# Optimization experiments

Measured on AMD Instinct MI355X. Metric: run time of the kernel, lower is better.

Reference implementation:

```python
import jax, jax.numpy as jnp
import numpy as np

EPS = 1e-08
ROUTING_ITERS = 3

def squash(s, axis=-1):
    norm = jnp.linalg.norm(s, axis=axis, keepdims=True)
    return norm / (1.0 + norm ** 2 + EPS) * s

def setup_inputs() -> dict:
    key = jax.random.key(0)
    k1, k2, k3 = jax.random.split(key, 3)
    B, R, C, O, I = 512, 640, 10, 16, 8
    x = jax.random.normal(k1, (B, R, I), dtype=jnp.float32)
    W = jax.random.normal(k2, (R, C, O, I), dtype=jnp.float32) * 0.01
    bias = jax.random.uniform(k3, (1, 1, C, O), dtype=jnp.float32) * 0.01
    return {"x": x, "W": W, "bias": bias}

def reference(x, W, bias):
    # u_hat[b,r,c,o] = sum_i W[r,c,o,i] * x[b,r,i]
    u_hat = jnp.einsum('rcoi,bri->brco', W, x)  # [B,R,C,O]
    u_hat_d = jax.lax.stop_gradient(u_hat)
    B, R, C, _ = u_hat.shape
    b_ij = jnp.zeros((B, R, C, 1), dtype=u_hat.dtype)
    v_j = None
    for itr in range(ROUTING_ITERS):
        c_ij = jax.nn.softmax(b_ij, axis=2)               # softmax over capsules
        s_j = jnp.sum(c_ij * u_hat_d, axis=1, keepdims=True) + bias  # [B,1,C,O]
        v_j = squash(s_j, axis=-1)
        if itr < ROUTING_ITERS - 1:
            a_ij = jnp.sum(u_hat * v_j, axis=-1, keepdims=True)  # agreement, non-detached
            b_ij = b_ij + a_ij
    return jnp.squeeze(v_j, axis=1)  # [B,C,O]
```

## Files before the change

### kernel.cpp

```cpp
#include <hip/hip_runtime.h>
#include <hip/hip_cooperative_groups.h>
#include <math.h>

namespace cg = cooperative_groups;

#define BB 512
#define RR 640
#define CC 10
#define OO 16
#define CO 160
#define II 8
#define S_FLOATS (BB*CO)

#define ZCH (RR*CO)
#define LSTR 165

#define CG_NRG 16
#define CG_RPW 10

#define FB_NRG 32
#define FB_RPW 5

using f16x8 = __attribute__((ext_vector_type(8))) _Float16;
using f32x4 = __attribute__((ext_vector_type(4))) float;



__device__ __forceinline__ float exp_small(float a) {
    float f = __builtin_fmaf(a, 0.16666667f, 0.5f);
    f = __builtin_fmaf(a, f, 1.0f);
    return __builtin_fmaf(a, f, 1.0f);
}

__device__ __forceinline__ float rowsum16(float v) {
    int t;
    t = __builtin_amdgcn_update_dpp(0, __float_as_int(v), 0x128, 0xF, 0xF, true);
    v += __int_as_float(t);
    t = __builtin_amdgcn_update_dpp(0, __float_as_int(v), 0x124, 0xF, 0xF, true);
    v += __int_as_float(t);
    t = __builtin_amdgcn_update_dpp(0, __float_as_int(v), 0x122, 0xF, 0xF, true);
    v += __int_as_float(t);
    t = __builtin_amdgcn_update_dpp(0, __float_as_int(v), 0x121, 0xF, 0xF, true);
    v += __int_as_float(t);
    return v;
}


__global__ __launch_bounds__(256) void prep(const float* __restrict__ W,
                                            const float* __restrict__ x,
                                            _Float16* __restrict__ wf,
                                            _Float16* __restrict__ xf) {
    const int t = blockIdx.x * 256 + threadIdx.x;
    if (t < RR * CO * II) wf[t] = (_Float16)W[t];
    if (t < 16) wf[RR * CO * II + t] = (_Float16)0.f;
    const int i = t & 7;
    const int b = (t >> 3) & 511;
    const int r = t >> 12;
    xf[t] = (_Float16)x[((size_t)b * RR + r) * II + i];
}


template <bool UNIFORM, int RPW_>
__device__ __forceinline__ void pass_tile(const _Float16* __restrict__ wf,
                                          const _Float16* __restrict__ xf,
                                          const float* __restrict__ vacc,
                                          float* __restrict__ part,
                                          float* __restrict__ red,
                                          int bt, int rg, int wv, int lane) {
    const int n  = lane & 15;
    const int q  = lane >> 4;
    const bool q0 = (q == 0);
    const int b0 = bt * 16;
    const int r0 = rg * (4 * RPW_) + wv * RPW_;

    const f16x8* xq = reinterpret_cast<const f16x8*>(xf);
    const int4*  wq = reinterpret_cast<const int4*>(wf);

    f32x4 sacc[CC];
#pragma unroll
    for (int c = 0; c < CC; ++c) sacc[c] = (f32x4){0.f, 0.f, 0.f, 0.f};

    if (UNIFORM) {
        int rr = 0;
#pragma unroll
        for (; rr + 4 <= RPW_; rr += 4) {
            const int r = r0 + rr + q;
            const f16x8 bfr = xq[(size_t)r * BB + b0 + n];
#pragma unroll
            for (int c = 0; c < CC; ++c) {
                const int4 a = wq[r * CO + c * 16 + n];
                sacc[c] = __builtin_amdgcn_mfma_f32_16x16x32_f16(
                    __builtin_bit_cast(f16x8, a), bfr, sacc[c], 0, 0, 0);
            }
        }
        constexpr int REM = RPW_ & 3;
        if (REM) {
            const int qq = (q < REM) ? q : 0;
            const int r = r0 + (RPW_ - REM) + qq;
            const f16x8 bfr = xq[(size_t)r * BB + b0 + n];
#pragma unroll
            for (int c = 0; c < CC; ++c) {
                const int4 a = wq[(q < REM) ? (r * CO + c * 16 + n) : ZCH];
                sacc[c] = __builtin_amdgcn_mfma_f32_16x16x32_f16(
                    __builtin_bit_cast(f16x8, a), bfr, sacc[c], 0, 0, 0);
            }
        }
    } else {
        f32x4 vv[CC];
        const f32x4* vp = reinterpret_cast<const f32x4*>(vacc + (size_t)(b0 + n) * CO);
#pragma unroll
        for (int c = 0; c < CC; ++c) vv[c] = vp[c * 4 + q];

#pragma unroll 2
        for (int rr = 0; rr < RPW_; ++rr) {
            const int r = r0 + rr;
            const f16x8 bcur = xq[(size_t)r * BB + b0 + n];

            f32x4 acc[CC];
#pragma unroll
            for (int c = 0; c < CC; ++c) {
                const int4 a = wq[q0 ? (r * CO + c * 16 + n) : ZCH];
                acc[c] = __builtin_amdgcn_mfma_f32_16x16x32_f16(
                    __builtin_bit_cast(f16x8, a), bcur,
                    (f32x4){0.f, 0.f, 0.f, 0.f}, 0, 0, 0);
            }

            float e[CC];
#pragma unroll
            for (int c = 0; c < CC; ++c) {
                float t = acc[c][0] * vv[c][0] + acc[c][1] * vv[c][1]
                        + acc[c][2] * vv[c][2] + acc[c][3] * vv[c][3];
                t += __shfl_xor(t, 16);
                t += __shfl_xor(t, 32);
                e[c] = exp_small(t);
            }
            const float se = (((e[0] + e[1]) + (e[2] + e[3]))
                            + ((e[4] + e[5]) + (e[6] + e[7]))) + (e[8] + e[9]);
            const float inv = __fdividef(1.0f, se);
#pragma unroll
            for (int c = 0; c < CC; ++c) {
                const float w = e[c] * inv;
#pragma unroll
                for (int k = 0; k < 4; ++k)
                    sacc[c][k] = __builtin_fmaf(w, acc[c][k], sacc[c][k]);
            }
        }
    }

    const int cb = 4 * q;
    if (wv < 2) {
        float* dst = red + ((wv * 16 + n) * LSTR + cb);
#pragma unroll
        for (int c = 0; c < CC; ++c)
#pragma unroll
            for (int k = 0; k < 4; ++k) dst[c * 16 + k] = sacc[c][k];
    }
    __syncthreads();
    if (wv >= 2) {
        float* dst = red + (((wv - 2) * 16 + n) * LSTR + cb);
#pragma unroll
        for (int c = 0; c < CC; ++c)
#pragma unroll
            for (int k = 0; k < 4; ++k) dst[c * 16 + k] += sacc[c][k];
    }
    __syncthreads();
    if (wv == 0) {
        const float f = UNIFORM ? 0.1f : 1.0f;
        float* pb = part + (size_t)rg * S_FLOATS + (size_t)(b0 + n) * CO + cb;
        const float* ra = red + (n * LSTR + cb);
        const float* rb = red + ((16 + n) * LSTR + cb);
#pragma unroll
        for (int c = 0; c < CC; ++c) {
            f32x4 v;
#pragma unroll
            for (int k = 0; k < 4; ++k)
                v[k] = (ra[c * 16 + k] + rb[c * 16 + k]) * f;
            *reinterpret_cast<f32x4*>(pb + c * 16) = v;
        }
    }
}

__device__ __forceinline__ void squash_elem(const float* __restrict__ part, int nsl,
                                            const float* __restrict__ bias,
                                            float* __restrict__ vacc,
                                            float* __restrict__ out,
                                            int mode, int idx) {
    const int co = idx % CO;
    float a0 = 0.f, a1 = 0.f, a2 = 0.f, a3 = 0.f;
    int s = 0;
    for (; s + 4 <= nsl; s += 4) {
        a0 += part[(size_t)s * S_FLOATS + idx];
        a1 += part[(size_t)(s + 1) * S_FLOATS + idx];
        a2 += part[(size_t)(s + 2) * S_FLOATS + idx];
        a3 += part[(size_t)(s + 3) * S_FLOATS + idx];
    }
    for (; s < nsl; ++s) a0 += part[(size_t)s * S_FLOATS + idx];
    const float val = ((a0 + a1) + (a2 + a3)) + bias[co];
    const float sq = rowsum16(val * val);
    const float norm  = sqrtf(sq);
    const float scale = norm / (1.0f + sq + 1e-8f);
    const float v = scale * val;
    if (mode == 0)      vacc[idx] = v;
    else if (mode == 1) vacc[idx] += v;
    else                out[idx] = v;
}

__global__ __launch_bounds__(256, 2) void caps_coop(const _Float16* __restrict__ wf,
                                                    const _Float16* __restrict__ xf,
                                                    float* __restrict__ vacc,
                                                    float* __restrict__ part,
                                                    const float* __restrict__ bias,
                                                    float* __restrict__ out) {
    __shared__ float red[2 * 16 * LSTR];
    cg::grid_group grid = cg::this_grid();
    const int tid  = threadIdx.x;
    const int lane = tid & 63;
    const int wv   = tid >> 6;
    const int bid  = blockIdx.x;
    const int bt   = bid & 31;
    const int rg   = bid >> 5;
    const int gth  = bid * 256 + tid;
    const bool sq_active = (gth < S_FLOATS);

    pass_tile<true, CG_RPW>(wf, xf, nullptr, part, red, bt, rg, wv, lane);
    grid.sync();
    if (sq_active) squash_elem(part, CG_NRG, bias, vacc, out, 0, gth);
    grid.sync();

    pass_tile<false, CG_RPW>(wf, xf, vacc, part, red, bt, rg, wv, lane);
    grid.sync();
    if (sq_active) squash_elem(part, CG_NRG, bias, vacc, out, 1, gth);
    grid.sync();

    pass_tile<false, CG_RPW>(wf, xf, vacc, part, red, bt, rg, wv, lane);
    grid.sync();
    if (sq_active) squash_elem(part, CG_NRG, bias, vacc, out, 2, gth);
}

template <bool UNIFORM>
__global__ __launch_bounds__(256, 2) void caps_pass_k(const _Float16* __restrict__ wf,
                                                      const _Float16* __restrict__ xf,
                                                      const float* __restrict__ vacc,
                                                      float* __restrict__ part) {
    __shared__ float red[2 * 16 * LSTR];
    pass_tile<UNIFORM, FB_RPW>(wf, xf, vacc, part, red,
                               blockIdx.x, blockIdx.y, threadIdx.x >> 6,
                               threadIdx.x & 63);
}

__global__ __launch_bounds__(256) void caps_squash_k(const float* __restrict__ part,
                                                     int nsl,
                                                     const float* __restrict__ bias,
                                                     float* __restrict__ vacc,
                                                     float* __restrict__ out,
                                                     int mode) {
    squash_elem(part, nsl, bias, vacc, out, mode, blockIdx.x * 256 + threadIdx.x);
}


extern "C" void kernel_launch(void* const* d_in, const int* in_sizes, int n_in,
                              void* d_out, int out_size, void* d_ws, size_t ws_size,
                              hipStream_t stream) {
    const float* x    = (const float*)d_in[0];
    const float* W    = (const float*)d_in[1];
    const float* bias = (const float*)d_in[2];
    float* out  = (float*)d_out;

    float*    part = (float*)d_ws;
    float*    vacc = part + (size_t)FB_NRG * S_FLOATS;
    _Float16* wf   = (_Float16*)(vacc + S_FLOATS);
    _Float16* xf   = wf + (size_t)RR * CO * II + 16;

    prep<<<BB * RR * II / 256, 256, 0, stream>>>(W, x, wf, xf);

    int maxB = 0;
    hipError_t qe = hipOccupancyMaxActiveBlocksPerMultiprocessor(
        &maxB, reinterpret_cast<const void*>(caps_coop), 256, 0);
    hipError_t le = hipErrorUnknown;
    if (qe == hipSuccess && maxB >= 2) {
        const _Float16* wfc = wf;
        const _Float16* xfc = xf;
        const float* biasc = bias;
        void* args[] = {(void*)&wfc, (void*)&xfc, (void*)&vacc,
                        (void*)&part, (void*)&biasc, (void*)&out};
        le = hipLaunchCooperativeKernel(reinterpret_cast<const void*>(caps_coop),
                                        dim3(512), dim3(256), args, 0, stream);
    }

    if (le != hipSuccess) {
        const dim3 pg(32, FB_NRG);
        const int sqg = S_FLOATS / 256;
        caps_pass_k<true><<<pg, 256, 0, stream>>>(wf, xf, nullptr, part);
        caps_squash_k<<<sqg, 256, 0, stream>>>(part, FB_NRG, bias, vacc, out, 0);
        caps_pass_k<false><<<pg, 256, 0, stream>>>(wf, xf, vacc, part);
        caps_squash_k<<<sqg, 256, 0, stream>>>(part, FB_NRG, bias, vacc, out, 1);
        caps_pass_k<false><<<pg, 256, 0, stream>>>(wf, xf, vacc, part);
        caps_squash_k<<<sqg, 256, 0, stream>>>(part, FB_NRG, bias, vacc, out, 2);
    }
}
```

Baseline: 134.6 us.

## Replace cooperative grid-sync kernel with separate pass/squash launches over 40 row groups

Drops the cooperative kernel, which synchronised the whole grid between routing passes, and instead launches distinct pass and squash kernels for each iteration. The route dimension is split into 40 groups of 16 rows, giving 1280 blocks, and the four waves of a block now interleave rows instead of each taking a contiguous chunk. Launch bounds rise to 5 blocks per CU for more occupancy. The cost is extra kernel launch overhead and more partial-sum traffic (40 slices) in the squash reduction. A smaller fallback with 8 groups is used when the workspace is too small.

```diff
diff --git a/kernel.cpp b/kernel.cpp
--- a/kernel.cpp
+++ b/kernel.cpp
@@ -1,8 +1,5 @@
 #include <hip/hip_runtime.h>
-#include <hip/hip_cooperative_groups.h>
 #include <math.h>
-
-namespace cg = cooperative_groups;
 
 #define BB 512
 #define RR 640
@@ -15,11 +12,10 @@
 #define ZCH (RR*CO)
 #define LSTR 165
 
-#define CG_NRG 16
-#define CG_RPW 10
-
-#define FB_NRG 32
-#define FB_RPW 5
+#define NRG    40
+#define RPB_MN (RR/NRG)
+#define NRG_FB 8
+#define RPB_FB (RR/NRG_FB)
 
 using f16x8 = __attribute__((ext_vector_type(8))) _Float16;
 using f32x4 = __attribute__((ext_vector_type(4))) float;
@@ -60,18 +56,21 @@
 }
 
 
-template <bool UNIFORM, int RPW_>
-__device__ __forceinline__ void pass_tile(const _Float16* __restrict__ wf,
-                                          const _Float16* __restrict__ xf,
-                                          const float* __restrict__ vacc,
-                                          float* __restrict__ part,
-                                          float* __restrict__ red,
-                                          int bt, int rg, int wv, int lane) {
-    const int n  = lane & 15;
-    const int q  = lane >> 4;
-    const bool q0 = (q == 0);
-    const int b0 = bt * 16;
-    const int r0 = rg * (4 * RPW_) + wv * RPW_;
+template <bool UNIFORM, int RPB_>
+__global__ __launch_bounds__(256, 5) void caps_pass(const _Float16* __restrict__ wf,
+                                                    const _Float16* __restrict__ xf,
+                                                    const float* __restrict__ vacc,
+                                                    float* __restrict__ part) {
+    __shared__ float red[2 * 16 * LSTR];
+    const int tid  = threadIdx.x;
+    const int lane = tid & 63;
+    const int wv   = tid >> 6;
+    const int n    = lane & 15;
+    const int q    = lane >> 4;
+    const bool q0  = (q == 0);
+    const int b0   = blockIdx.x * 16;
+    const int rg   = blockIdx.y;
+    const int r0   = rg * RPB_;
 
     const f16x8* xq = reinterpret_cast<const f16x8*>(xf);
     const int4*  wq = reinterpret_cast<const int4*>(wf);
@@ -81,26 +80,13 @@
     for (int c = 0; c < CC; ++c) sacc[c] = (f32x4){0.f, 0.f, 0.f, 0.f};
 
     if (UNIFORM) {
-        int rr = 0;
-#pragma unroll
-        for (; rr + 4 <= RPW_; rr += 4) {
+#pragma unroll
+        for (int rr = 4 * wv; rr + 4 <= RPB_; rr += 16) {
             const int r = r0 + rr + q;
             const f16x8 bfr = xq[(size_t)r * BB + b0 + n];
 #pragma unroll
             for (int c = 0; c < CC; ++c) {
                 const int4 a = wq[r * CO + c * 16 + n];
-                sacc[c] = __builtin_amdgcn_mfma_f32_16x16x32_f16(
-                    __builtin_bit_cast(f16x8, a), bfr, sacc[c], 0, 0, 0);
-            }
-        }
-        constexpr int REM = RPW_ & 3;
-        if (REM) {
-            const int qq = (q < REM) ? q : 0;
-            const int r = r0 + (RPW_ - REM) + qq;
-            const f16x8 bfr = xq[(size_t)r * BB + b0 + n];
-#pragma unroll
-            for (int c = 0; c < CC; ++c) {
-                const int4 a = wq[(q < REM) ? (r * CO + c * 16 + n) : ZCH];
                 sacc[c] = __builtin_amdgcn_mfma_f32_16x16x32_f16(
                     __builtin_bit_cast(f16x8, a), bfr, sacc[c], 0, 0, 0);
             }
@@ -111,8 +97,8 @@
 #pragma unroll
         for (int c = 0; c < CC; ++c) vv[c] = vp[c * 4 + q];
 
-#pragma unroll 2
-        for (int rr = 0; rr < RPW_; ++rr) {
+#pragma unroll
+        for (int rr = wv; rr < RPB_; rr += 4) {
             const int r = r0 + rr;
             const f16x8 bcur = xq[(size_t)r * BB + b0 + n];
 
@@ -180,12 +166,14 @@
     }
 }
 
-__device__ __forceinline__ void squash_elem(const float* __restrict__ part, int nsl,
-                                            const float* __restrict__ bias,
-                                            float* __restrict__ vacc,
-                                            float* __restrict__ out,
-                                            int mode, int idx) {
-    const int co = idx % CO;
+__global__ __launch_bounds__(256) void caps_squash(const float* __restrict__ part,
+                                                   int nsl,
+                                                   const float* __restrict__ bias,
+                                                   float* __restrict__ vacc,
+                                                   float* __restrict__ out,
+                                                   int mode) {
+    const int idx = blockIdx.x * 256 + threadIdx.x;
+    const int co  = idx % CO;
     float a0 = 0.f, a1 = 0.f, a2 = 0.f, a3 = 0.f;
     int s = 0;
     for (; s + 4 <= nsl; s += 4) {
@@ -205,58 +193,6 @@
     else                out[idx] = v;
 }
 
-__global__ __launch_bounds__(256, 2) void caps_coop(const _Float16* __restrict__ wf,
-                                                    const _Float16* __restrict__ xf,
-                                                    float* __restrict__ vacc,
-                                                    float* __restrict__ part,
-                                                    const float* __restrict__ bias,
-                                                    float* __restrict__ out) {
-    __shared__ float red[2 * 16 * LSTR];
-    cg::grid_group grid = cg::this_grid();
-    const int tid  = threadIdx.x;
-    const int lane = tid & 63;
-    const int wv   = tid >> 6;
-    const int bid  = blockIdx.x;
-    const int bt   = bid & 31;
-    const int rg   = bid >> 5;
-    const int gth  = bid * 256 + tid;
-    const bool sq_active = (gth < S_FLOATS);
-
-    pass_tile<true, CG_RPW>(wf, xf, nullptr, part, red, bt, rg, wv, lane);
-    grid.sync();
-    if (sq_active) squash_elem(part, CG_NRG, bias, vacc, out, 0, gth);
-    grid.sync();
-
-    pass_tile<false, CG_RPW>(wf, xf, vacc, part, red, bt, rg, wv, lane);
-    grid.sync();
-    if (sq_active) squash_elem(part, CG_NRG, bias, vacc, out, 1, gth);
-    grid.sync();
-
-    pass_tile<false, CG_RPW>(wf, xf, vacc, part, red, bt, rg, wv, lane);
-    grid.sync();
-    if (sq_active) squash_elem(part, CG_NRG, bias, vacc, out, 2, gth);
-}
-
-template <bool UNIFORM>
-__global__ __launch_bounds__(256, 2) void caps_pass_k(const _Float16* __restrict__ wf,
-                                                      const _Float16* __restrict__ xf,
-                                                      const float* __restrict__ vacc,
-                                                      float* __restrict__ part) {
-    __shared__ float red[2 * 16 * LSTR];
-    pass_tile<UNIFORM, FB_RPW>(wf, xf, vacc, part, red,
-                               blockIdx.x, blockIdx.y, threadIdx.x >> 6,
-                               threadIdx.x & 63);
-}
-
-__global__ __launch_bounds__(256) void caps_squash_k(const float* __restrict__ part,
-                                                     int nsl,
-                                                     const float* __restrict__ bias,
-                                                     float* __restrict__ vacc,
-                                                     float* __restrict__ out,
-                                                     int mode) {
-    squash_elem(part, nsl, bias, vacc, out, mode, blockIdx.x * 256 + threadIdx.x);
-}
-
 
 extern "C" void kernel_launch(void* const* d_in, const int* in_sizes, int n_in,
                               void* d_out, int out_size, void* d_ws, size_t ws_size,
@@ -266,35 +202,38 @@
     const float* bias = (const float*)d_in[2];
     float* out  = (float*)d_out;
 
+    const int sqg = S_FLOATS / 256;
+
     float*    part = (float*)d_ws;
-    float*    vacc = part + (size_t)FB_NRG * S_FLOATS;
+    float*    vacc = part + (size_t)NRG * S_FLOATS;
     _Float16* wf   = (_Float16*)(vacc + S_FLOATS);
     _Float16* xf   = wf + (size_t)RR * CO * II + 16;
 
-    prep<<<BB * RR * II / 256, 256, 0, stream>>>(W, x, wf, xf);
-
-    int maxB = 0;
-    hipError_t qe = hipOccupancyMaxActiveBlocksPerMultiprocessor(
-        &maxB, reinterpret_cast<const void*>(caps_coop), 256, 0);
-    hipError_t le = hipErrorUnknown;
-    if (qe == hipSuccess && maxB >= 2) {
-        const _Float16* wfc = wf;
-        const _Float16* xfc = xf;
-        const float* biasc = bias;
-        void* args[] = {(void*)&wfc, (void*)&xfc, (void*)&vacc,
-                        (void*)&part, (void*)&biasc, (void*)&out};
-        le = hipLaunchCooperativeKernel(reinterpret_cast<const void*>(caps_coop),
-                                        dim3(512), dim3(256), args, 0, stream);
-    }
-
-    if (le != hipSuccess) {
-        const dim3 pg(32, FB_NRG);
-        const int sqg = S_FLOATS / 256;
-        caps_pass_k<true><<<pg, 256, 0, stream>>>(wf, xf, nullptr, part);
-        caps_squash_k<<<sqg, 256, 0, stream>>>(part, FB_NRG, bias, vacc, out, 0);
-        caps_pass_k<false><<<pg, 256, 0, stream>>>(wf, xf, vacc, part);
-        caps_squash_k<<<sqg, 256, 0, stream>>>(part, FB_NRG, bias, vacc, out, 1);
-        caps_pass_k<false><<<pg, 256, 0, stream>>>(wf, xf, vacc, part);
-        caps_squash_k<<<sqg, 256, 0, stream>>>(part, FB_NRG, bias, vacc, out, 2);
-    }
-}
+    const size_t NEEDED = ((size_t)NRG + 1) * S_FLOATS * 4
+                        + ((size_t)RR * CO * II + 16) * 2
+                        + (size_t)BB * RR * II * 2;
+
+    if (ws_size >= NEEDED) {
+        prep<<<BB * RR * II / 256, 256, 0, stream>>>(W, x, wf, xf);
+        const dim3 pg(32, NRG);
+        caps_pass<true,  RPB_MN><<<pg, 256, 0, stream>>>(wf, xf, nullptr, part);
+        caps_squash<<<sqg, 256, 0, stream>>>(part, NRG, bias, vacc, out, 0);
+        caps_pass<false, RPB_MN><<<pg, 256, 0, stream>>>(wf, xf, vacc, part);
+        caps_squash<<<sqg, 256, 0, stream>>>(part, NRG, bias, vacc, out, 1);
+        caps_pass<false, RPB_MN><<<pg, 256, 0, stream>>>(wf, xf, vacc, part);
+        caps_squash<<<sqg, 256, 0, stream>>>(part, NRG, bias, vacc, out, 2);
+    } else {
+        float*    partf = (float*)d_ws;
+        float*    vaccf = partf + (size_t)NRG_FB * S_FLOATS;
+        _Float16* wff   = (_Float16*)(vaccf + S_FLOATS);
+        _Float16* xff   = wff + (size_t)RR * CO * II + 16;
+        prep<<<BB * RR * II / 256, 256, 0, stream>>>(W, x, wff, xff);
+        const dim3 pg(32, NRG_FB);
+        caps_pass<true,  RPB_FB><<<pg, 256, 0, stream>>>(wff, xff, nullptr, partf);
+        caps_squash<<<sqg, 256, 0, stream>>>(partf, NRG_FB, bias, vaccf, out, 0);
+        caps_pass<false, RPB_FB><<<pg, 256, 0, stream>>>(wff, xff, vaccf, partf);
+        caps_squash<<<sqg, 256, 0, stream>>>(partf, NRG_FB, bias, vaccf, out, 1);
+        caps_pass<false, RPB_FB><<<pg, 256, 0, stream>>>(wff, xff, vaccf, partf);
+        caps_squash<<<sqg, 256, 0, stream>>>(partf, NRG_FB, bias, vaccf, out, 2);
+    }
+}
```

Result: slower. 214.9 us (+59.6%).

## Materialize fp16 u_hat once and reuse it across routing iterations

Applied to the files above, without the earlier changes.

The first pass now computes u_hat with MFMA and writes it to workspace as fp16 in a lane-ready layout. Later routing passes reload it instead of recomputing the matmul, and v is staged in shared memory. The grid grows to 1280 blocks at 5 per CU with 16 rows per block, which raises occupancy and adds more partial slices for the squash step to reduce. The trade is extra global traffic for the u_hat buffer, about 105MB written and read twice, plus a larger reduction over 40 slices.

```diff
diff --git a/kernel.cpp b/kernel.cpp
--- a/kernel.cpp
+++ b/kernel.cpp
@@ -7,19 +7,17 @@
 #define BB 512
 #define RR 640
 #define CC 10
-#define OO 16
 #define CO 160
 #define II 8
 #define S_FLOATS (BB*CO)
 
+#define NRG 40
+#define RPB 16
 #define ZCH (RR*CO)
 #define LSTR 165
-
-#define CG_NRG 16
-#define CG_RPW 10
-
-#define FB_NRG 32
-#define FB_RPW 5
+#define VSTR 164
+#define VOFF 5280
+#define SMEM_FLOATS (VOFF + 16*VSTR)
 
 using f16x8 = __attribute__((ext_vector_type(8))) _Float16;
 using f32x4 = __attribute__((ext_vector_type(4))) float;
@@ -45,108 +43,9 @@
     return v;
 }
 
-
-__global__ __launch_bounds__(256) void prep(const float* __restrict__ W,
-                                            const float* __restrict__ x,
-                                            _Float16* __restrict__ wf,
-                                            _Float16* __restrict__ xf) {
-    const int t = blockIdx.x * 256 + threadIdx.x;
-    if (t < RR * CO * II) wf[t] = (_Float16)W[t];
-    if (t < 16) wf[RR * CO * II + t] = (_Float16)0.f;
-    const int i = t & 7;
-    const int b = (t >> 3) & 511;
-    const int r = t >> 12;
-    xf[t] = (_Float16)x[((size_t)b * RR + r) * II + i];
-}
-
-
-template <bool UNIFORM, int RPW_>
-__device__ __forceinline__ void pass_tile(const _Float16* __restrict__ wf,
-                                          const _Float16* __restrict__ xf,
-                                          const float* __restrict__ vacc,
-                                          float* __restrict__ part,
-                                          float* __restrict__ red,
-                                          int bt, int rg, int wv, int lane) {
-    const int n  = lane & 15;
-    const int q  = lane >> 4;
-    const bool q0 = (q == 0);
-    const int b0 = bt * 16;
-    const int r0 = rg * (4 * RPW_) + wv * RPW_;
-
-    const f16x8* xq = reinterpret_cast<const f16x8*>(xf);
-    const int4*  wq = reinterpret_cast<const int4*>(wf);
-
-    f32x4 sacc[CC];
-#pragma unroll
-    for (int c = 0; c < CC; ++c) sacc[c] = (f32x4){0.f, 0.f, 0.f, 0.f};
-
-    if (UNIFORM) {
-        int rr = 0;
-#pragma unroll
-        for (; rr + 4 <= RPW_; rr += 4) {
-            const int r = r0 + rr + q;
-            const f16x8 bfr = xq[(size_t)r * BB + b0 + n];
-#pragma unroll
-            for (int c = 0; c < CC; ++c) {
-                const int4 a = wq[r * CO + c * 16 + n];
-                sacc[c] = __builtin_amdgcn_mfma_f32_16x16x32_f16(
-                    __builtin_bit_cast(f16x8, a), bfr, sacc[c], 0, 0, 0);
-            }
-        }
-        constexpr int REM = RPW_ & 3;
-        if (REM) {
-            const int qq = (q < REM) ? q : 0;
-            const int r = r0 + (RPW_ - REM) + qq;
-            const f16x8 bfr = xq[(size_t)r * BB + b0 + n];
-#pragma unroll
-            for (int c = 0; c < CC; ++c) {
-                const int4 a = wq[(q < REM) ? (r * CO + c * 16 + n) : ZCH];
-                sacc[c] = __builtin_amdgcn_mfma_f32_16x16x32_f16(
-                    __builtin_bit_cast(f16x8, a), bfr, sacc[c], 0, 0, 0);
-            }
-        }
-    } else {
-        f32x4 vv[CC];
-        const f32x4* vp = reinterpret_cast<const f32x4*>(vacc + (size_t)(b0 + n) * CO);
-#pragma unroll
-        for (int c = 0; c < CC; ++c) vv[c] = vp[c * 4 + q];
-
-#pragma unroll 2
-        for (int rr = 0; rr < RPW_; ++rr) {
-            const int r = r0 + rr;
-            const f16x8 bcur = xq[(size_t)r * BB + b0 + n];
-
-            f32x4 acc[CC];
-#pragma unroll
-            for (int c = 0; c < CC; ++c) {
-                const int4 a = wq[q0 ? (r * CO + c * 16 + n) : ZCH];
-                acc[c] = __builtin_amdgcn_mfma_f32_16x16x32_f16(
-                    __builtin_bit_cast(f16x8, a), bcur,
-                    (f32x4){0.f, 0.f, 0.f, 0.f}, 0, 0, 0);
-            }
-
-            float e[CC];
-#pragma unroll
-            for (int c = 0; c < CC; ++c) {
-                float t = acc[c][0] * vv[c][0] + acc[c][1] * vv[c][1]
-                        + acc[c][2] * vv[c][2] + acc[c][3] * vv[c][3];
-                t += __shfl_xor(t, 16);
-                t += __shfl_xor(t, 32);
-                e[c] = exp_small(t);
-            }
-            const float se = (((e[0] + e[1]) + (e[2] + e[3]))
-                            + ((e[4] + e[5]) + (e[6] + e[7]))) + (e[8] + e[9]);
-            const float inv = __fdividef(1.0f, se);
-#pragma unroll
-            for (int c = 0; c < CC; ++c) {
-                const float w = e[c] * inv;
-#pragma unroll
-                for (int k = 0; k < 4; ++k)
-                    sacc[c][k] = __builtin_fmaf(w, acc[c][k], sacc[c][k]);
-            }
-        }
-    }
-
+__device__ __forceinline__ void block_reduce_store(f32x4* sacc, float* red,
+                                                   float* part, int rg, int b0,
+                                                   int wv, int n, int q, float f) {
     const int cb = 4 * q;
     if (wv < 2) {
         float* dst = red + ((wv * 16 + n) * LSTR + cb);
@@ -165,7 +64,6 @@
     }
     __syncthreads();
     if (wv == 0) {
-        const float f = UNIFORM ? 0.1f : 1.0f;
         float* pb = part + (size_t)rg * S_FLOATS + (size_t)(b0 + n) * CO + cb;
         const float* ra = red + (n * LSTR + cb);
         const float* rb = red + ((16 + n) * LSTR + cb);
@@ -205,47 +103,215 @@
     else                out[idx] = v;
 }
 
-__global__ __launch_bounds__(256, 2) void caps_coop(const _Float16* __restrict__ wf,
-                                                    const _Float16* __restrict__ xf,
-                                                    float* __restrict__ vacc,
-                                                    float* __restrict__ part,
-                                                    const float* __restrict__ bias,
-                                                    float* __restrict__ out) {
-    __shared__ float red[2 * 16 * LSTR];
+
+__global__ __launch_bounds__(256) void prep(const float* __restrict__ W,
+                                            const float* __restrict__ x,
+                                            _Float16* __restrict__ wf,
+                                            _Float16* __restrict__ xf) {
+    const int t = blockIdx.x * 256 + threadIdx.x;
+    if (t < RR * CO * II) wf[t] = (_Float16)W[t];
+    if (t < 16) wf[RR * CO * II + t] = (_Float16)0.f;
+    const int i = t & 7;
+    const int b = (t >> 3) & 511;
+    const int r = t >> 12;
+    xf[t] = (_Float16)x[((size_t)b * RR + r) * II + i];
+}
+
+
+__global__ __launch_bounds__(256, 5) void caps_all(const _Float16* __restrict__ wf,
+                                                   const _Float16* __restrict__ xf,
+                                                   _Float16* __restrict__ u,
+                                                   float* __restrict__ vacc,
+                                                   float* __restrict__ part,
+                                                   const float* __restrict__ bias,
+                                                   float* __restrict__ out) {
+    __shared__ float smem[SMEM_FLOATS];
     cg::grid_group grid = cg::this_grid();
     const int tid  = threadIdx.x;
     const int lane = tid & 63;
     const int wv   = tid >> 6;
+    const int n    = lane & 15;
+    const int q    = lane >> 4;
+    const bool q0  = (q == 0);
     const int bid  = blockIdx.x;
     const int bt   = bid & 31;
     const int rg   = bid >> 5;
+    const int b0   = bt * 16;
+    const int r0   = rg * RPB;
     const int gth  = bid * 256 + tid;
-    const bool sq_active = (gth < S_FLOATS);
-
-    pass_tile<true, CG_RPW>(wf, xf, nullptr, part, red, bt, rg, wv, lane);
+    const bool sqa = (gth < S_FLOATS);
+
+    const f16x8* xq = reinterpret_cast<const f16x8*>(xf);
+    const int4*  wq = reinterpret_cast<const int4*>(wf);
+    int4*        uq = reinterpret_cast<int4*>(u);
+
+    {
+        f32x4 sacc[CC];
+#pragma unroll
+        for (int c = 0; c < CC; ++c) sacc[c] = (f32x4){0.f, 0.f, 0.f, 0.f};
+
+#pragma unroll 2
+        for (int j = 0; j < 4; ++j) {
+            const int r = r0 + wv * 4 + j;
+            const f16x8 bfr = xq[(size_t)r * BB + b0 + n];
+#pragma unroll
+            for (int p = 0; p < 5; ++p) {
+                const int4 a0 = wq[q0 ? (r * CO + (2 * p) * 16 + n) : ZCH];
+                const int4 a1 = wq[q0 ? (r * CO + (2 * p + 1) * 16 + n) : ZCH];
+                const f32x4 acc0 = __builtin_amdgcn_mfma_f32_16x16x32_f16(
+                    __builtin_bit_cast(f16x8, a0), bfr, (f32x4){0.f,0.f,0.f,0.f}, 0,0,0);
+                const f32x4 acc1 = __builtin_amdgcn_mfma_f32_16x16x32_f16(
+                    __builtin_bit_cast(f16x8, a1), bfr, (f32x4){0.f,0.f,0.f,0.f}, 0,0,0);
+                f16x8 uo;
+#pragma unroll
+                for (int k = 0; k < 4; ++k) {
+                    uo[k]     = (_Float16)acc0[k];
+                    uo[4 + k] = (_Float16)acc1[k];
+                }
+                uq[(((size_t)r * 32 + bt) * 5 + p) * 64 + lane] =
+                    __builtin_bit_cast(int4, uo);
+#pragma unroll
+                for (int k = 0; k < 4; ++k) {
+                    sacc[2 * p][k]     += acc0[k];
+                    sacc[2 * p + 1][k] += acc1[k];
+                }
+            }
+        }
+        block_reduce_store(sacc, smem, part, rg, b0, wv, n, q, 0.1f);
+    }
     grid.sync();
-    if (sq_active) squash_elem(part, CG_NRG, bias, vacc, out, 0, gth);
+    if (sqa) squash_elem(part, NRG, bias, vacc, out, 0, gth);
     grid.sync();
 
-    pass_tile<false, CG_RPW>(wf, xf, vacc, part, red, bt, rg, wv, lane);
-    grid.sync();
-    if (sq_active) squash_elem(part, CG_NRG, bias, vacc, out, 1, gth);
-    grid.sync();
-
-    pass_tile<false, CG_RPW>(wf, xf, vacc, part, red, bt, rg, wv, lane);
-    grid.sync();
-    if (sq_active) squash_elem(part, CG_NRG, bias, vacc, out, 2, gth);
-}
+#pragma unroll 1
+    for (int it = 1; it <= 2; ++it) {
+        {
+            const float4* vg = reinterpret_cast<const float4*>(vacc);
+            for (int k2 = tid; k2 < 640; k2 += 256) {
+                const int bl = k2 / 40, ch = k2 - bl * 40;
+                *reinterpret_cast<float4*>(smem + VOFF + bl * VSTR + ch * 4) =
+                    vg[(size_t)(b0 + bl) * 40 + ch];
+            }
+        }
+        __syncthreads();
+        const float* vb = smem + VOFF + n * VSTR + 4 * q;
+
+        f32x4 sacc[CC];
+#pragma unroll
+        for (int c = 0; c < CC; ++c) sacc[c] = (f32x4){0.f, 0.f, 0.f, 0.f};
+
+#pragma unroll 2
+        for (int j = 0; j < 4; ++j) {
+            const int r = r0 + wv * 4 + j;
+            int4 uc[5];
+#pragma unroll
+            for (int p = 0; p < 5; ++p)
+                uc[p] = uq[(((size_t)r * 32 + bt) * 5 + p) * 64 + lane];
+
+            float e[CC];
+#pragma unroll
+            for (int c = 0; c < CC; ++c) {
+                const f16x8 h = __builtin_bit_cast(f16x8, uc[c >> 1]);
+                const int bs = (c & 1) * 4;
+                const f32x4 vvc = *reinterpret_cast<const f32x4*>(vb + c * 16);
+                float t = (float)h[bs] * vvc[0] + (float)h[bs + 1] * vvc[1]
+                        + (float)h[bs + 2] * vvc[2] + (float)h[bs + 3] * vvc[3];
+                t += __shfl_xor(t, 16);
+                t += __shfl_xor(t, 32);
+                e[c] = exp_small(t);
+            }
+            const float se = (((e[0] + e[1]) + (e[2] + e[3]))
+                            + ((e[4] + e[5]) + (e[6] + e[7]))) + (e[8] + e[9]);
+            const float inv = __fdividef(1.0f, se);
+#pragma unroll
+            for (int c = 0; c < CC; ++c) {
+                const float w = e[c] * inv;
+                const f16x8 h = __builtin_bit_cast(f16x8, uc[c >> 1]);
+                const int bs = (c & 1) * 4;
+#pragma unroll
+                for (int k = 0; k < 4; ++k)
+                    sacc[c][k] = __builtin_fmaf(w, (float)h[bs + k], sacc[c][k]);
+            }
+        }
+        block_reduce_store(sacc, smem, part, rg, b0, wv, n, q, 1.0f);
+        grid.sync();
+        if (sqa) squash_elem(part, NRG, bias, vacc, out, it, gth);
+        if (it == 1) grid.sync();
+    }
+}
+
 
 template <bool UNIFORM>
-__global__ __launch_bounds__(256, 2) void caps_pass_k(const _Float16* __restrict__ wf,
-                                                      const _Float16* __restrict__ xf,
-                                                      const float* __restrict__ vacc,
-                                                      float* __restrict__ part) {
+__global__ __launch_bounds__(256) void caps_pass_g(const _Float16* __restrict__ wf,
+                                                   const _Float16* __restrict__ xf,
+                                                   const float* __restrict__ vacc,
+                                                   float* __restrict__ part) {
     __shared__ float red[2 * 16 * LSTR];
-    pass_tile<UNIFORM, FB_RPW>(wf, xf, vacc, part, red,
-                               blockIdx.x, blockIdx.y, threadIdx.x >> 6,
-                               threadIdx.x & 63);
+    const int tid  = threadIdx.x;
+    const int lane = tid & 63;
+    const int wv   = tid >> 6;
+    const int n    = lane & 15;
+    const int q    = lane >> 4;
+    const bool q0  = (q == 0);
+    const int b0   = blockIdx.x * 16;
+    const int rg   = blockIdx.y;
+    const int r0   = rg * RPB;
+
+    const f16x8* xq = reinterpret_cast<const f16x8*>(xf);
+    const int4*  wq = reinterpret_cast<const int4*>(wf);
+
+    f32x4 sacc[CC];
+#pragma unroll
+    for (int c = 0; c < CC; ++c) sacc[c] = (f32x4){0.f, 0.f, 0.f, 0.f};
+
+    if (UNIFORM) {
+        const int r = r0 + 4 * wv + q;
+        const f16x8 bfr = xq[(size_t)r * BB + b0 + n];
+#pragma unroll
+        for (int c = 0; c < CC; ++c) {
+            const int4 a = wq[r * CO + c * 16 + n];
+            sacc[c] = __builtin_amdgcn_mfma_f32_16x16x32_f16(
+                __builtin_bit_cast(f16x8, a), bfr, sacc[c], 0, 0, 0);
+        }
+    } else {
+        f32x4 vv[CC];
+        const f32x4* vp = reinterpret_cast<const f32x4*>(vacc + (size_t)(b0 + n) * CO);
+#pragma unroll
+        for (int c = 0; c < CC; ++c) vv[c] = vp[c * 4 + q];
+#pragma unroll 2
+        for (int rr = wv; rr < RPB; rr += 4) {
+            const int r = r0 + rr;
+            const f16x8 bcur = xq[(size_t)r * BB + b0 + n];
+            f32x4 acc[CC];
+#pragma unroll
+            for (int c = 0; c < CC; ++c) {
+                const int4 a = wq[q0 ? (r * CO + c * 16 + n) : ZCH];
+                acc[c] = __builtin_amdgcn_mfma_f32_16x16x32_f16(
+                    __builtin_bit_cast(f16x8, a), bcur,
+                    (f32x4){0.f, 0.f, 0.f, 0.f}, 0, 0, 0);
+            }
+            float e[CC];
+#pragma unroll
+            for (int c = 0; c < CC; ++c) {
+                float t = acc[c][0] * vv[c][0] + acc[c][1] * vv[c][1]
+                        + acc[c][2] * vv[c][2] + acc[c][3] * vv[c][3];
+                t += __shfl_xor(t, 16);
+                t += __shfl_xor(t, 32);
+                e[c] = exp_small(t);
+            }
+            const float se = (((e[0] + e[1]) + (e[2] + e[3]))
+                            + ((e[4] + e[5]) + (e[6] + e[7]))) + (e[8] + e[9]);
+            const float inv = __fdividef(1.0f, se);
+#pragma unroll
+            for (int c = 0; c < CC; ++c) {
+                const float w = e[c] * inv;
+#pragma unroll
+                for (int k = 0; k < 4; ++k)
+                    sacc[c][k] = __builtin_fmaf(w, acc[c][k], sacc[c][k]);
+            }
+        }
+    }
+    block_reduce_store(sacc, red, part, rg, b0, wv, n, q, UNIFORM ? 0.1f : 1.0f);
 }
 
 __global__ __launch_bounds__(256) void caps_squash_k(const float* __restrict__ part,
@@ -266,35 +332,47 @@
     const float* bias = (const float*)d_in[2];
     float* out  = (float*)d_out;
 
+    const int sqg = S_FLOATS / 256;
+
     float*    part = (float*)d_ws;
-    float*    vacc = part + (size_t)FB_NRG * S_FLOATS;
+    float*    vacc = part + (size_t)NRG * S_FLOATS;
     _Float16* wf   = (_Float16*)(vacc + S_FLOATS);
     _Float16* xf   = wf + (size_t)RR * CO * II + 16;
+    _Float16* uu   = xf + (size_t)BB * RR * II;
+
+    const size_t NEED_FB = ((size_t)NRG + 1) * S_FLOATS * 4
+                         + ((size_t)RR * CO * II + 16) * 2
+                         + (size_t)BB * RR * II * 2;
+    const size_t NEED_CO = NEED_FB + (size_t)RR * BB * CO * 2;
 
     prep<<<BB * RR * II / 256, 256, 0, stream>>>(W, x, wf, xf);
 
-    int maxB = 0;
-    hipError_t qe = hipOccupancyMaxActiveBlocksPerMultiprocessor(
-        &maxB, reinterpret_cast<const void*>(caps_coop), 256, 0);
-    hipError_t le = hipErrorUnknown;
-    if (qe == hipSuccess && maxB >= 2) {
-        const _Float16* wfc = wf;
-        const _Float16* xfc = xf;
-        const float* biasc = bias;
-        void* args[] = {(void*)&wfc, (void*)&xfc, (void*)&vacc,
-                        (void*)&part, (void*)&biasc, (void*)&out};
-        le = hipLaunchCooperativeKernel(reinterpret_cast<const void*>(caps_coop),
-                                        dim3(512), dim3(256), args, 0, stream);
-    }
-
-    if (le != hipSuccess) {
-        const dim3 pg(32, FB_NRG);
-        const int sqg = S_FLOATS / 256;
-        caps_pass_k<true><<<pg, 256, 0, stream>>>(wf, xf, nullptr, part);
-        caps_squash_k<<<sqg, 256, 0, stream>>>(part, FB_NRG, bias, vacc, out, 0);
-        caps_pass_k<false><<<pg, 256, 0, stream>>>(wf, xf, vacc, part);
-        caps_squash_k<<<sqg, 256, 0, stream>>>(part, FB_NRG, bias, vacc, out, 1);
-        caps_pass_k<false><<<pg, 256, 0, stream>>>(wf, xf, vacc, part);
-        caps_squash_k<<<sqg, 256, 0, stream>>>(part, FB_NRG, bias, vacc, out, 2);
-    }
-}
+    bool launched = false;
+    if (ws_size >= NEED_CO) {
+        int maxB = 0;
+        hipError_t qe = hipOccupancyMaxActiveBlocksPerMultiprocessor(
+            &maxB, reinterpret_cast<const void*>(caps_all), 256, 0);
+        if (qe == hipSuccess && maxB >= 5) {
+            const _Float16* wfc = wf;
+            const _Float16* xfc = xf;
+            _Float16* uc = uu;
+            const float* bc = bias;
+            void* args[] = {(void*)&wfc, (void*)&xfc, (void*)&uc,
+                            (void*)&vacc, (void*)&part, (void*)&bc, (void*)&out};
+            hipError_t le = hipLaunchCooperativeKernel(
+                reinterpret_cast<const void*>(caps_all),
+                dim3(32 * NRG), dim3(256), args, 0, stream);
+            launched = (le == hipSuccess);
+        }
+    }
+
+    if (!launched) {
+        const dim3 pg(32, NRG);
+        caps_pass_g<true ><<<pg, 256, 0, stream>>>(wf, xf, nullptr, part);
+        caps_squash_k<<<sqg, 256, 0, stream>>>(part, NRG, bias, vacc, out, 0);
+        caps_pass_g<false><<<pg, 256, 0, stream>>>(wf, xf, vacc, part);
+        caps_squash_k<<<sqg, 256, 0, stream>>>(part, NRG, bias, vacc, out, 1);
+        caps_pass_g<false><<<pg, 256, 0, stream>>>(wf, xf, vacc, part);
+        caps_squash_k<<<sqg, 256, 0, stream>>>(part, NRG, bias, vacc, out, 2);
+    }
+}
```

Result: no change. 137.0 us (+1.7%).
